# Performance work log

Measured on AMD Instinct MI355X. Metric: run time of the kernel, lower is better.

Reference implementation:

```python
import jax, jax.numpy as jnp
import numpy as np

B, S, DIM = 1, 2048, 1024
HEADS, KV_HEADS, DH = 16, 2, 64
GQ = HEADS // KV_HEADS
CBS = 64   # compress block size
SBS = 64   # selection block size
NUM_SEL = 8
WIN = 512  # sliding window size
NUM_MEM = 1
SCALE = DH ** -0.5
NEG = -jnp.finfo(jnp.float32).max


def setup_inputs():
    ks = jax.random.split(jax.random.key(0), 12)
    cdim = CBS * DH
    dim_inner = HEADS * DH
    dim_kv = KV_HEADS * DH
    p = lambda k, shape: jax.random.normal(k, shape, jnp.float32) * 0.02
    return {
        "x": jax.random.normal(ks[0], (B, S, DIM), jnp.float32),
        "rms_g": jnp.ones((DIM,), jnp.float32),
        "W_qkv": p(ks[1], (DIM, dim_inner + 2 * dim_kv)),
        "k_pos": p(ks[2], (KV_HEADS, CBS, DH)),
        "v_pos": p(ks[3], (KV_HEADS, CBS, DH)),
        "mem_kv": p(ks[4], (2, KV_HEADS, NUM_MEM, DH)),
        "kW1": p(ks[5], (cdim, cdim)), "kb1": jnp.zeros((cdim,), jnp.float32),
        "kW2": p(ks[6], (cdim, DH)), "kb2": jnp.zeros((DH,), jnp.float32),
        "vW1": p(ks[7], (cdim, cdim)), "vb1": jnp.zeros((cdim,), jnp.float32),
        "vW2": p(ks[8], (cdim, DH)), "vb2": jnp.zeros((DH,), jnp.float32),
        "W_comb": p(ks[9], (DIM, 3 * HEADS)),
        "b_comb": jnp.tile(jnp.array([-2.0, -2.0, 2.0], jnp.float32), HEADS),
        "W_out": p(ks[10], (HEADS * DH, DIM)),
    }


def _rot_half(u):
    v = u.reshape(u.shape[:-1] + (DH // 2, 2))
    return jnp.stack([-v[..., 1], v[..., 0]], axis=-1).reshape(u.shape)


def reference(x, rms_g, W_qkv, k_pos, v_pos, mem_kv, kW1, kb1, kW2, kb2,
              vW1, vb1, vW2, vb2, W_comb, b_comb, W_out):
    n_cb = S // CBS
    n_fb = S // SBS
    num_sel = min(NUM_SEL, n_cb)

    # RMSNorm
    xn = x * jax.lax.rsqrt(jnp.mean(x * x, -1, keepdims=True) + jnp.finfo(jnp.float32).eps) * rms_g

    qkv = xn @ W_qkv
    q, k, v = jnp.split(qkv, [HEADS * DH, (HEADS + KV_HEADS) * DH], axis=-1)
    q = q.reshape(B, S, HEADS, DH).transpose(0, 2, 1, 3)       # b h n d
    k = k.reshape(B, S, KV_HEADS, DH).transpose(0, 2, 1, 3)
    v = v.reshape(B, S, KV_HEADS, DH).transpose(0, 2, 1, 3)

    # ---- compressed branch: per-block MLP compression of K/V ----
    kc = (k + jnp.tile(k_pos, (1, n_cb, 1))[None]).reshape(B, KV_HEADS, n_cb, CBS * DH)
    vc = (v + jnp.tile(v_pos, (1, n_cb, 1))[None]).reshape(B, KV_HEADS, n_cb, CBS * DH)
    ck = jax.nn.relu(kc @ kW1 + kb1) @ kW2 + kb2               # b h w d
    cv = jax.nn.relu(vc @ vW1 + vb1) @ vW2 + vb2
    ck = jnp.concatenate([jnp.broadcast_to(mem_kv[0], (B, KV_HEADS, NUM_MEM, DH)), ck], axis=2)
    cv = jnp.concatenate([jnp.broadcast_to(mem_kv[1], (B, KV_HEADS, NUM_MEM, DH)), cv], axis=2)
    ck_seq = jnp.concatenate([jnp.full((NUM_MEM,), -1), (jnp.arange(n_cb) + 1) * CBS - 1])
    cmask = ck_seq[None, :] < jnp.arange(S)[:, None]           # [S, mem+n_cb]
    qg = q.reshape(B, KV_HEADS, GQ, S, DH)
    csim = jnp.einsum('bhgid,bhjd->bhgij', qg, ck) * SCALE
    csim = jnp.where(cmask, csim, NEG)
    c_out = jnp.einsum('bhgij,bhjd->bhgid', jax.nn.softmax(csim, -1), cv).reshape(B, HEADS, S, DH)

    # ---- rotary embedding (interleaved pairs, theta=10000) ----
    inv_freq = 1.0 / (10000.0 ** (jnp.arange(0, DH, 2, dtype=jnp.float32) / DH))
    freqs = jnp.repeat(jnp.arange(S, dtype=jnp.float32)[:, None] * inv_freq, 2, axis=-1)
    cos, sin = jnp.cos(freqs), jnp.sin(freqs)
    rq = q * cos + _rot_half(q) * sin
    rk = k * cos + _rot_half(k) * sin

    # ---- block selection from compressed attention scores ----
    imp = csim[..., NUM_MEM:].mean(axis=2)                     # mean over grouped queries: [B,KVH,S,n_cb]
    imp = jnp.concatenate([jnp.full(imp.shape[:-1] + (1,), -1000.0), imp], -1)
    imp = jax.nn.softmax(imp, -1)[..., 1:]
    sel_val, sel_idx = jax.lax.top_k(imp, num_sel)             # [B,KVH,S,sel]
    fmask = jnp.broadcast_to((sel_val > 1e-10)[..., None], (B, KV_HEADS, S, num_sel, SBS))
    diag_idx = jnp.broadcast_to((jnp.arange(S) // SBS)[None, None, :, None], (B, KV_HEADS, S, 1))
    sel_idx = jnp.concatenate([sel_idx, diag_idx], -1)         # append own (diagonal) block
    causal = jnp.tril(jnp.ones((SBS, SBS), bool))
    diag_mask = jnp.broadcast_to(jnp.tile(causal, (n_fb, 1))[None, None, :, None, :], (B, KV_HEADS, S, 1, SBS))
    fmask = jnp.concatenate([fmask, diag_mask], axis=-2).reshape(B, KV_HEADS, S, (num_sel + 1) * SBS)

    # ---- fine attention over gathered selected blocks ----
    fkb = rk.reshape(B, KV_HEADS, 1, n_fb, SBS, DH)
    fvb = v.reshape(B, KV_HEADS, 1, n_fb, SBS, DH)
    gi = sel_idx[..., None, None]                              # [B,KVH,S,sel+1,1,1]
    fk = jnp.take_along_axis(fkb, gi, axis=3).reshape(B, KV_HEADS, S, (num_sel + 1) * SBS, DH)
    fv = jnp.take_along_axis(fvb, gi, axis=3).reshape(B, KV_HEADS, S, (num_sel + 1) * SBS, DH)
    fqg = rq.reshape(B, KV_HEADS, GQ, S, DH)
    fsim = jnp.einsum('bhgid,bhijd->bhgij', fqg, fk) * SCALE
    fsim = jnp.where(fmask[:, :, None], fsim, NEG)
    f_out = jnp.einsum('bhgij,bhijd->bhgid', jax.nn.softmax(fsim, -1), fv).reshape(B, HEADS, S, DH)

    # ---- causal sliding window (exact window, look_backward=1) ----
    skf = jnp.repeat(rk, GQ, axis=1)
    svf = jnp.repeat(v, GQ, axis=1)
    nw = S // WIN
    kw = skf.reshape(B, HEADS, nw, WIN, DH)
    vw = svf.reshape(B, HEADS, nw, WIN, DH)
    kcat = jnp.concatenate([jnp.pad(kw, ((0, 0), (0, 0), (1, 0), (0, 0), (0, 0)))[:, :, :nw], kw], axis=3)
    vcat = jnp.concatenate([jnp.pad(vw, ((0, 0), (0, 0), (1, 0), (0, 0), (0, 0)))[:, :, :nw], vw], axis=3)
    qw = rq.reshape(B, HEADS, nw, WIN, DH)
    gq_pos = jnp.arange(nw)[:, None, None] * WIN + jnp.arange(WIN)[None, :, None]
    gk_pos = jnp.arange(nw)[:, None, None] * WIN - WIN + jnp.arange(2 * WIN)[None, None, :]
    smask = (gk_pos >= 0) & (gk_pos <= gq_pos) & (gq_pos - gk_pos <= WIN)
    ssim = jnp.where(smask, jnp.einsum('bhwid,bhwjd->bhwij', qw, kcat) * SCALE, NEG)
    s_out = jnp.einsum('bhwij,bhwjd->bhwid', jax.nn.softmax(ssim, -1), vcat).reshape(B, HEADS, S, DH)

    # ---- learned per-token, per-head strategy combination ----
    gates = jax.nn.sigmoid(xn @ W_comb + b_comb).reshape(B, S, HEADS, 3).transpose(0, 2, 1, 3)
    out = gates[..., 0:1] * c_out + gates[..., 1:2] * f_out + gates[..., 2:3] * s_out
    return out.transpose(0, 2, 1, 3).reshape(B, S, HEADS * DH) @ W_out
```

## Files before the change

kernel.cpp:

```cpp
#include <hip/hip_runtime.h>
#include <hip/hip_bf16.h>
#include <cstddef>
#include <cstdint>

#define S      2048
#define DIM    1024
#define HEADS  16
#define KVH    2
#define GQ     8
#define DH     64
#define CBS    64
#define SBS    64
#define NUMSEL 8
#define WIN    512
#define NCB    (S / CBS)
#define CDIM   (CBS * DH)
#define QKVC   (HEADS * DH + 2 * KVH * DH)
#define KOFF   (HEADS * DH)
#define VOFF   (HEADS * DH + KVH * DH)
#define SCALE  0.125f
#define RMS_EPS 1.1920928955078125e-07f

typedef __attribute__((ext_vector_type(8))) short bf16x8;
typedef __attribute__((ext_vector_type(4))) float f32x4;

__device__ inline short f2bs(float f) {
    __hip_bfloat16 b = __float2bfloat16(f);
    return *(short*)&b;
}

__device__ inline float wave_sum(float v) {
    for (int o = 32; o > 0; o >>= 1) v += __shfl_xor(v, o);
    return v;
}

__global__ __launch_bounds__(256) void rmsnorm_kernel(
        const float* __restrict__ x, const float* __restrict__ g,
        float* __restrict__ xn, __hip_bfloat16* __restrict__ xnb) {
    int s = blockIdx.x, tid = threadIdx.x;
    const float4* row = (const float4*)(x + (size_t)s * DIM);
    float4 v = row[tid];
    float ss = v.x * v.x + v.y * v.y + v.z * v.z + v.w * v.w;
    ss = wave_sum(ss);
    __shared__ float red[4];
    if ((tid & 63) == 0) red[tid >> 6] = ss;
    __syncthreads();
    float tot = red[0] + red[1] + red[2] + red[3];
    float sc = rsqrtf(tot / (float)DIM + RMS_EPS);
    float4 gg = ((const float4*)g)[tid];
    float4 o;
    o.x = v.x * sc * gg.x; o.y = v.y * sc * gg.y;
    o.z = v.z * sc * gg.z; o.w = v.w * sc * gg.w;
    ((float4*)(xn + (size_t)s * DIM))[tid] = o;
    size_t b = (size_t)s * DIM + tid * 4;
    xnb[b + 0] = __float2bfloat16(o.x);
    xnb[b + 1] = __float2bfloat16(o.y);
    xnb[b + 2] = __float2bfloat16(o.z);
    xnb[b + 3] = __float2bfloat16(o.w);
}

__global__ __launch_bounds__(256) void cast_bf16_kernel(
        const float* __restrict__ in, __hip_bfloat16* __restrict__ out, int n4) {
    int e = blockIdx.x * 256 + threadIdx.x;
    if (e >= n4) return;
    float4 v = ((const float4*)in)[e];
    out[4 * e + 0] = __float2bfloat16(v.x);
    out[4 * e + 1] = __float2bfloat16(v.y);
    out[4 * e + 2] = __float2bfloat16(v.z);
    out[4 * e + 3] = __float2bfloat16(v.w);
}

__global__ __launch_bounds__(256) void transpose_cast_kernel(
        const float* __restrict__ W, short* __restrict__ Wt, int K, int N) {
    __shared__ float tile[64][65];
    int n0 = blockIdx.x * 64, k0 = blockIdx.y * 64;
    int tid = threadIdx.x;
    #pragma unroll
    for (int e = 0; e < 16; e++) {
        int idx = tid + e * 256;
        int r = idx >> 6, c = idx & 63;
        float v = 0.f;
        if (n0 + c < N) v = W[(size_t)(k0 + r) * N + n0 + c];
        tile[r][c] = v;
    }
    __syncthreads();
    #pragma unroll
    for (int e = 0; e < 16; e++) {
        int idx = tid + e * 256;
        int r = idx >> 6, c = idx & 63;
        if (n0 + r < N)
            Wt[(size_t)(n0 + r) * K + k0 + c] = f2bs(tile[c][r]);
    }
}

__global__ __launch_bounds__(256) void cast_v_kernel(
        const float* __restrict__ qkv, short* __restrict__ vb) {
    int e = blockIdx.x * 256 + threadIdx.x;
    if (e >= S * KVH * DH / 4) return;
    int idx = e * 4;
    int tok = idx / (KVH * DH), rem = idx % (KVH * DH);
    float4 v = *(const float4*)(qkv + (size_t)tok * QKVC + VOFF + rem);
    vb[idx + 0] = f2bs(v.x);
    vb[idx + 1] = f2bs(v.y);
    vb[idx + 2] = f2bs(v.z);
    vb[idx + 3] = f2bs(v.w);
}

template <int BM, int BN, int WM, int WN, int ACT>
__global__ __launch_bounds__(256) void gemm_bt_kernel(
        const __hip_bfloat16* __restrict__ A, const short* __restrict__ Bt,
        const float* __restrict__ bias, float* __restrict__ C,
        int M, int N, int K) {
    constexpr int BK = 32;
    constexpr int TM = BM / (WM * 16);
    constexpr int TN = BN / (WN * 16);
    constexpr int LDK = BK + 8;
    __shared__ short As[BM][LDK];
    __shared__ short Bs[BN][LDK];
    int tid = threadIdx.x;
    int wave = tid >> 6, lane = tid & 63;
    int wm = wave % WM, wn = wave / WM;
    int m0 = wm * TM * 16, n0 = wn * TN * 16;
    int bm = blockIdx.y * BM, bn = blockIdx.x * BN;
    int lm = lane & 15, quad = lane >> 4;
    const short* Ash = (const short*)A;
    f32x4 acc[TM][TN] = {};
    for (int k0 = 0; k0 < K; k0 += BK) {
        #pragma unroll
        for (int e = 0; e < BM * BK / (256 * 8); e++) {
            int idx = (tid + e * 256) * 8;
            int r = idx >> 5, kk = idx & 31;
            *(bf16x8*)(&As[r][kk]) =
                *(const bf16x8*)(Ash + (size_t)(bm + r) * K + k0 + kk);
        }
        #pragma unroll
        for (int e = 0; e < BN * BK / (256 * 8); e++) {
            int idx = (tid + e * 256) * 8;
            int r = idx >> 5, kk = idx & 31;
            bf16x8 v = {};
            if (bn + r < N)
                v = *(const bf16x8*)(Bt + (size_t)(bn + r) * K + k0 + kk);
            *(bf16x8*)(&Bs[r][kk]) = v;
        }
        __syncthreads();
        bf16x8 af[TM], bf_[TN];
        #pragma unroll
        for (int i = 0; i < TM; i++)
            af[i] = *(const bf16x8*)(&As[m0 + i * 16 + lm][quad * 8]);
        #pragma unroll
        for (int j = 0; j < TN; j++)
            bf_[j] = *(const bf16x8*)(&Bs[n0 + j * 16 + lm][quad * 8]);
        #pragma unroll
        for (int i = 0; i < TM; i++)
            #pragma unroll
            for (int j = 0; j < TN; j++)
                acc[i][j] = __builtin_amdgcn_mfma_f32_16x16x32_bf16(
                    af[i], bf_[j], acc[i][j], 0, 0, 0);
        __syncthreads();
    }
    #pragma unroll
    for (int i = 0; i < TM; i++) {
        #pragma unroll
        for (int j = 0; j < TN; j++) {
            int gn = bn + n0 + j * 16 + lm;
            if (gn >= N) continue;
            #pragma unroll
            for (int r = 0; r < 4; r++) {
                int gm = bm + m0 + i * 16 + quad * 4 + r;
                float v = acc[i][j][r];
                if (bias) v += bias[gn];
                if (ACT == 2) v = 1.f / (1.f + expf(-v));
                C[(size_t)gm * N + gn] = v;
            }
        }
    }
}

template <int BM, int BN, int WM, int WN>
__global__ __launch_bounds__(256) void gemm_mfma_kernel(
        const __hip_bfloat16* __restrict__ A, const float* __restrict__ B,
        float* __restrict__ C, int M, int N, int K, int kslice) {
    constexpr int BK = 32;
    constexpr int TM = BM / (WM * 16);
    constexpr int TN = BN / (WN * 16);
    constexpr int LDK = BK + 8;
    constexpr int NB = BN * BK / 256;
    __shared__ __hip_bfloat16 As[BM][LDK];
    __shared__ __hip_bfloat16 Bs[BN][LDK];
    int tid = threadIdx.x;
    int wave = tid >> 6, lane = tid & 63;
    int wm = wave % WM, wn = wave / WM;
    int m0 = wm * TM * 16, n0 = wn * TN * 16;
    int bm = blockIdx.y * BM, bn = blockIdx.x * BN;
    int kbeg = blockIdx.z * kslice, kend = kbeg + kslice;
    int lm = lane & 15, quad = lane >> 4;
    f32x4 acc[TM][TN] = {};
    for (int k0 = kbeg; k0 < kend; k0 += BK) {
        #pragma unroll
        for (int e = 0; e < BM * BK / (256 * 8); e++) {
            int idx = (tid + e * 256) * 8;
            int r = idx >> 5, kk = idx & 31;
            *(bf16x8*)(&As[r][kk]) =
                *(const bf16x8*)(A + (size_t)(bm + r) * K + k0 + kk);
        }
        float tmpB[NB];
        #pragma unroll
        for (int e = 0; e < NB; e++) {
            int idx = tid + e * 256;
            int kk = idx / BN, n = idx % BN;
            tmpB[e] = B[(size_t)(k0 + kk) * N + bn + n];
        }
        #pragma unroll
        for (int e = 0; e < NB; e++) {
            int idx = tid + e * 256;
            int kk = idx / BN, n = idx % BN;
            Bs[n][kk] = __float2bfloat16(tmpB[e]);
        }
        __syncthreads();
        bf16x8 af[TM], bf_[TN];
        #pragma unroll
        for (int i = 0; i < TM; i++)
            af[i] = *(const bf16x8*)(&As[m0 + i * 16 + lm][quad * 8]);
        #pragma unroll
        for (int j = 0; j < TN; j++)
            bf_[j] = *(const bf16x8*)(&Bs[n0 + j * 16 + lm][quad * 8]);
        #pragma unroll
        for (int i = 0; i < TM; i++)
            #pragma unroll
            for (int j = 0; j < TN; j++)
                acc[i][j] = __builtin_amdgcn_mfma_f32_16x16x32_bf16(
                    af[i], bf_[j], acc[i][j], 0, 0, 0);
        __syncthreads();
    }
    size_t cbase = (size_t)blockIdx.z * M * N;
    #pragma unroll
    for (int i = 0; i < TM; i++) {
        #pragma unroll
        for (int j = 0; j < TN; j++) {
            int gn = bn + n0 + j * 16 + lm;
            #pragma unroll
            for (int r = 0; r < 4; r++) {
                int gm = bm + m0 + i * 16 + quad * 4 + r;
                C[cbase + (size_t)gm * N + gn] = acc[i][j][r];
            }
        }
    }
}

__global__ __launch_bounds__(256) void gemm_splitk_kernel(
        const float* __restrict__ A, const float* __restrict__ B,
        float* __restrict__ P, int M, int N, int K, int kslice) {
    const int BM = 64, BN = 64, BK = 16;
    __shared__ float As[BK][BM + 4];
    __shared__ float Bs[BK][BN];
    int bm = blockIdx.y * BM, bn = blockIdx.x * BN;
    int z = blockIdx.z;
    int kbeg = z * kslice, kend = kbeg + kslice;
    int tid = threadIdx.x;
    int tx = tid & 15, ty = tid >> 4;
    float acc[4][4] = {{0.f}};
    for (int k0 = kbeg; k0 < kend; k0 += BK) {
        #pragma unroll
        for (int e = 0; e < 4; e++) {
            int idx = tid + e * 256;
            int m = idx >> 4, kk = idx & 15;
            int gm = bm + m;
            As[kk][m] = (gm < M) ? A[(size_t)gm * K + k0 + kk] : 0.f;
        }
        #pragma unroll
        for (int e = 0; e < 4; e++) {
            int idx = tid + e * 256;
            int kk = idx >> 6, n = idx & 63;
            int gn = bn + n;
            Bs[kk][n] = (gn < N) ? B[(size_t)(k0 + kk) * N + gn] : 0.f;
        }
        __syncthreads();
        #pragma unroll
        for (int kk = 0; kk < BK; kk++) {
            float a[4], b[4];
            #pragma unroll
            for (int i = 0; i < 4; i++) a[i] = As[kk][ty * 4 + i];
            #pragma unroll
            for (int j = 0; j < 4; j++) b[j] = Bs[kk][tx * 4 + j];
            #pragma unroll
            for (int i = 0; i < 4; i++)
                #pragma unroll
                for (int j = 0; j < 4; j++) acc[i][j] += a[i] * b[j];
        }
        __syncthreads();
    }
    #pragma unroll
    for (int i = 0; i < 4; i++) {
        int gm = bm + ty * 4 + i;
        if (gm >= M) continue;
        #pragma unroll
        for (int j = 0; j < 4; j++) {
            int gn = bn + tx * 4 + j;
            if (gn >= N) continue;
            P[((size_t)z * M + gm) * N + gn] = acc[i][j];
        }
    }
}

template <int ACT>
__global__ __launch_bounds__(256) void reduce_splitk_kernel(
        const float* __restrict__ P, const float* __restrict__ bias,
        float* __restrict__ C, int MN, int N, int splits) {
    int e = blockIdx.x * 256 + threadIdx.x;
    if (e >= MN) return;
    float s = 0.f;
    for (int z = 0; z < splits; z++) s += P[(size_t)z * MN + e];
    s += bias[e % N];
    if (ACT == 1) s = fmaxf(s, 0.f);
    C[e] = s;
}

__global__ __launch_bounds__(256) void rotary_kernel(
        const float* __restrict__ qkv, short* __restrict__ rqb, short* __restrict__ rkb) {
    int s = blockIdx.x, tid = threadIdx.x;
    for (int p = tid; p < (HEADS + KVH) * (DH / 2); p += 256) {
        int t; const float* src; short* dst;
        if (p < HEADS * (DH / 2)) {
            int h = p >> 5; t = p & 31;
            src = qkv + (size_t)s * QKVC + h * DH + 2 * t;
            dst = rqb + (size_t)s * (HEADS * DH) + h * DH + 2 * t;
        } else {
            int pp = p - HEADS * (DH / 2);
            int h = pp >> 5; t = pp & 31;
            src = qkv + (size_t)s * QKVC + KOFF + h * DH + 2 * t;
            dst = rkb + (size_t)s * (KVH * DH) + h * DH + 2 * t;
        }
        float u0 = src[0], u1 = src[1];
        float freq = powf(10000.f, -((float)(2 * t) / (float)DH));
        float ang = (float)s * freq;
        float sn, cs;
        sincosf(ang, &sn, &cs);
        dst[0] = f2bs(u0 * cs - u1 * sn);
        dst[1] = f2bs(u1 * cs + u0 * sn);
    }
}

__global__ __launch_bounds__(256) void build_cmat_kernel(
        const float* __restrict__ qkv, const float* __restrict__ k_pos,
        const float* __restrict__ v_pos, __hip_bfloat16* __restrict__ kcm,
        __hip_bfloat16* __restrict__ vcm) {
    int r = blockIdx.x;
    int h = r >> 5, w = r & 31;
    for (int e = threadIdx.x; e < CDIM; e += 256) {
        int i = e >> 6, d = e & 63;
        size_t qb = (size_t)(w * CBS + i) * QKVC;
        kcm[(size_t)r * CDIM + e] =
            __float2bfloat16(qkv[qb + KOFF + h * DH + d] + k_pos[(h * CBS + i) * DH + d]);
        vcm[(size_t)r * CDIM + e] =
            __float2bfloat16(qkv[qb + VOFF + h * DH + d] + v_pos[(h * CBS + i) * DH + d]);
    }
}

__global__ __launch_bounds__(256) void assemble_kernel(
        const float* __restrict__ ckb, const float* __restrict__ cvb,
        const float* __restrict__ mem_kv, float* __restrict__ ck, float* __restrict__ cv,
        short* __restrict__ ck16, short* __restrict__ cv16) {
    int e = blockIdx.x * 256 + threadIdx.x;
    if (e >= KVH * (NCB + 1) * DH) return;
    int d = e & 63;
    int j = (e >> 6) % (NCB + 1);
    int h = e / ((NCB + 1) * DH);
    float kv, vv;
    if (j == 0) {
        kv = mem_kv[0 * KVH * DH + h * DH + d];
        vv = mem_kv[1 * KVH * DH + h * DH + d];
    } else {
        kv = ckb[((size_t)h * NCB + j - 1) * DH + d];
        vv = cvb[((size_t)h * NCB + j - 1) * DH + d];
    }
    ck[e] = kv; cv[e] = vv;
    ck16[e] = f2bs(kv); cv16[e] = f2bs(vv);
}

__global__ __launch_bounds__(64) void imp_kernel(
        const float* __restrict__ qkv, const float* __restrict__ ck,
        float* __restrict__ imp) {
    int kvh = blockIdx.x, s = blockIdx.y, t = threadIdx.x;
    __shared__ float qg[GQ * DH];
    __shared__ float ckl[NCB * 65];
    for (int e = t; e < GQ * DH; e += 64) {
        int g = e >> 6, d = e & 63;
        qg[e] = qkv[(size_t)s * QKVC + (kvh * GQ + g) * DH + d];
    }
    for (int e = t; e < NCB * DH; e += 64) {
        int w = e >> 6, d = e & 63;
        ckl[w * 65 + d] = ck[((size_t)kvh * (NCB + 1) + 1 + w) * DH + d];
    }
    __syncthreads();
    if (t < NCB) {
        int w = t;
        float val;
        if (w * CBS + CBS - 1 < s) {
            float acc = 0.f;
            #pragma unroll
            for (int g = 0; g < GQ; g++) {
                const float* qp = qg + g * DH;
                const float* cp = ckl + w * 65;
                #pragma unroll 16
                for (int d = 0; d < DH; d++) acc += qp[d] * cp[d];
            }
            val = acc * SCALE * (1.f / (float)GQ);
        } else {
            val = -INFINITY;
        }
        imp[((size_t)kvh * S + s) * NCB + w] = val;
    }
}

__global__ __launch_bounds__(256) void select_kernel(
        const float* __restrict__ imp, int* __restrict__ sel) {
    int idx = blockIdx.x * 256 + threadIdx.x;
    if (idx >= KVH * S) return;
    const float* row = imp + (size_t)idx * NCB;
    float p[NCB];
    float m = -1000.f;
    for (int w = 0; w < NCB; w++) { p[w] = row[w]; m = fmaxf(m, p[w]); }
    float z = expf(-1000.f - m);
    for (int w = 0; w < NCB; w++) { p[w] = expf(p[w] - m); z += p[w]; }
    float inv = 1.f / z;
    bool used[NCB];
    for (int w = 0; w < NCB; w++) used[w] = false;
    for (int i = 0; i < NUMSEL; i++) {
        int best = 0; float bv = -1.f;
        for (int w = 0; w < NCB; w++) {
            if (!used[w]) {
                float pw = p[w] * inv;
                if (pw > bv) { bv = pw; best = w; }
            }
        }
        used[best] = true;
        sel[(size_t)idx * NUMSEL + i] = (bv > 1e-10f) ? best : -1;
    }
}

__global__ __launch_bounds__(256) void cattn_kernel(
        const float* __restrict__ qkv, const short* __restrict__ ck16,
        const short* __restrict__ cv16, const float* __restrict__ gates,
        float* __restrict__ attn) {
    int h = blockIdx.x, qb = blockIdx.y;
    int kvh = h >> 3;
    int tid = threadIdx.x;
    int wv = tid >> 6, lane = tid & 63;
    int lm = lane & 15, quad = lane >> 4;
    __shared__ short Qb[64][72];
    __shared__ short Ks[64][72];
    __shared__ short Vt[64][72];
    __shared__ short Pb[64][72];
    for (int e = tid; e < 1024; e += 256) {
        int q = e >> 4, d4 = (e & 15) * 4;
        float4 v = *(const float4*)(qkv + (size_t)(qb * 64 + q) * QKVC + h * DH + d4);
        Qb[q][d4 + 0] = f2bs(v.x); Qb[q][d4 + 1] = f2bs(v.y);
        Qb[q][d4 + 2] = f2bs(v.z); Qb[q][d4 + 3] = f2bs(v.w);
    }
    for (int e = tid; e < 512; e += 256) {
        int c8 = e >> 6, j = e & 63;
        bf16x8 kv = {}, vv = {};
        if (j < NCB + 1) {
            kv = *(const bf16x8*)(ck16 + ((size_t)kvh * (NCB + 1) + j) * DH + c8 * 8);
            vv = *(const bf16x8*)(cv16 + ((size_t)kvh * (NCB + 1) + j) * DH + c8 * 8);
        }
        #pragma unroll
        for (int t = 0; t < 8; t++) {
            Ks[j][c8 * 8 + t] = kv[t];
            Vt[c8 * 8 + t][j] = vv[t];
        }
    }
    __syncthreads();
    bf16x8 aq0 = *(const bf16x8*)&Qb[wv * 16 + lm][quad * 8];
    bf16x8 aq1 = *(const bf16x8*)&Qb[wv * 16 + lm][32 + quad * 8];
    int vismax = (qb < NCB) ? qb : NCB;
    f32x4 sc[4];
    #pragma unroll
    for (int t = 0; t < 4; t++) {
        bf16x8 bk0 = *(const bf16x8*)&Ks[t * 16 + lm][quad * 8];
        bf16x8 bk1 = *(const bf16x8*)&Ks[t * 16 + lm][32 + quad * 8];
        f32x4 s4 = {0.f, 0.f, 0.f, 0.f};
        s4 = __builtin_amdgcn_mfma_f32_16x16x32_bf16(aq0, bk0, s4, 0, 0, 0);
        s4 = __builtin_amdgcn_mfma_f32_16x16x32_bf16(aq1, bk1, s4, 0, 0, 0);
        sc[t] = s4;
    }
    float l[4];
    float pr[4][4];
    #pragma unroll
    for (int r = 0; r < 4; r++) {
        float mx = -INFINITY;
        #pragma unroll
        for (int t = 0; t < 4; t++) {
            int jj = t * 16 + lm;
            bool vis = (jj == 0) || (jj <= vismax);
            float v = vis ? sc[t][r] * SCALE : -INFINITY;
            sc[t][r] = v;
            mx = fmaxf(mx, v);
        }
        #pragma unroll
        for (int o = 1; o < 16; o <<= 1) mx = fmaxf(mx, __shfl_xor(mx, o));
        float sum = 0.f;
        #pragma unroll
        for (int t = 0; t < 4; t++) {
            float p = expf(sc[t][r] - mx);
            pr[r][t] = p;
            sum += p;
        }
        #pragma unroll
        for (int o = 1; o < 16; o <<= 1) sum += __shfl_xor(sum, o);
        l[r] = sum;
    }
    #pragma unroll
    for (int r = 0; r < 4; r++)
        #pragma unroll
        for (int t = 0; t < 4; t++)
            Pb[wv * 16 + quad * 4 + r][t * 16 + lm] = f2bs(pr[r][t]);
    __syncthreads();
    bf16x8 ap0 = *(const bf16x8*)&Pb[wv * 16 + lm][quad * 8];
    bf16x8 ap1 = *(const bf16x8*)&Pb[wv * 16 + lm][32 + quad * 8];
    f32x4 oacc[4];
    #pragma unroll
    for (int t = 0; t < 4; t++) {
        bf16x8 bv0 = *(const bf16x8*)&Vt[t * 16 + lm][quad * 8];
        bf16x8 bv1 = *(const bf16x8*)&Vt[t * 16 + lm][32 + quad * 8];
        f32x4 a = {0.f, 0.f, 0.f, 0.f};
        a = __builtin_amdgcn_mfma_f32_16x16x32_bf16(ap0, bv0, a, 0, 0, 0);
        a = __builtin_amdgcn_mfma_f32_16x16x32_bf16(ap1, bv1, a, 0, 0, 0);
        oacc[t] = a;
    }
    #pragma unroll
    for (int r = 0; r < 4; r++) {
        int spos = qb * 64 + wv * 16 + quad * 4 + r;
        float g0 = gates[((size_t)spos * HEADS + h) * 3 + 0];
        float f = g0 / l[r];
        #pragma unroll
        for (int t = 0; t < 4; t++)
            attn[(size_t)spos * (HEADS * DH) + h * DH + t * 16 + lm] = oacc[t][r] * f;
    }
}

__global__ __launch_bounds__(64, 4) void fattn_kernel(
        const short* __restrict__ rqb, const short* __restrict__ rkb,
        const short* __restrict__ vb, const int* __restrict__ sel,
        const float* __restrict__ gates, float* __restrict__ attn) {
    int kvh = blockIdx.x, s = blockIdx.y;
    int lane = threadIdx.x;
    int lm = lane & 15, quad = lane >> 4;
    __shared__ short Vt[64][68];
    __shared__ short Pb[16][68];
    const short* qp = rqb + (size_t)s * (HEADS * DH) + (size_t)(kvh * 8 + (lm & 7)) * DH;
    bf16x8 aq0 = *(const bf16x8*)(qp + quad * 8);
    bf16x8 aq1 = *(const bf16x8*)(qp + 32 + quad * 8);
    int bl[9];
    {
        const int4* sp = (const int4*)(sel + ((size_t)kvh * S + s) * NUMSEL);
        int4 s0 = sp[0], s1 = sp[1];
        bl[0] = s0.x; bl[1] = s0.y; bl[2] = s0.z; bl[3] = s0.w;
        bl[4] = s1.x; bl[5] = s1.y; bl[6] = s1.z; bl[7] = s1.w;
        bl[8] = s >> 6;
    }
    float m[4], l[4];
    f32x4 oacc[4];
    #pragma unroll
    for (int r = 0; r < 4; r++) {
        m[r] = -INFINITY; l[r] = 0.f;
        oacc[r] = (f32x4){0.f, 0.f, 0.f, 0.f};
    }
    for (int i = 0; i < 9; i++) {
        int w = bl[i];
        if (i < NUMSEL && w < 0) continue;
        const short* vp = vb + ((size_t)(w * SBS + lane) * KVH + kvh) * DH;
        bf16x8 vv[8];
        #pragma unroll
        for (int r = 0; r < 8; r++) vv[r] = *(const bf16x8*)(vp + r * 8);
        f32x4 sc[4];
        #pragma unroll
        for (int t = 0; t < 4; t++) {
            const short* kp = rkb + ((size_t)(w * SBS + t * 16 + lm) * KVH + kvh) * DH;
            bf16x8 bk0 = *(const bf16x8*)(kp + quad * 8);
            bf16x8 bk1 = *(const bf16x8*)(kp + 32 + quad * 8);
            f32x4 s4 = {0.f, 0.f, 0.f, 0.f};
            s4 = __builtin_amdgcn_mfma_f32_16x16x32_bf16(aq0, bk0, s4, 0, 0, 0);
            s4 = __builtin_amdgcn_mfma_f32_16x16x32_bf16(aq1, bk1, s4, 0, 0, 0);
            sc[t] = s4;
        }
        #pragma unroll
        for (int r = 0; r < 8; r++)
            #pragma unroll
            for (int t = 0; t < 8; t++) Vt[r * 8 + t][lane] = vv[r][t];
        float pr[4][4];
        bool diag = (i == NUMSEL);
        #pragma unroll
        for (int r = 0; r < 4; r++) {
            float mx = -INFINITY;
            #pragma unroll
            for (int t = 0; t < 4; t++) {
                int jj = t * 16 + lm;
                bool vis = !diag || (jj <= (s & 63));
                float v = vis ? sc[t][r] * SCALE : -INFINITY;
                sc[t][r] = v;
                mx = fmaxf(mx, v);
            }
            #pragma unroll
            for (int o = 1; o < 16; o <<= 1) mx = fmaxf(mx, __shfl_xor(mx, o));
            float mn = fmaxf(m[r], mx);
            float al = __expf(m[r] - mn);
            float sum = 0.f;
            #pragma unroll
            for (int t = 0; t < 4; t++) {
                float p = __expf(sc[t][r] - mn);
                pr[r][t] = p;
                sum += p;
            }
            #pragma unroll
            for (int o = 1; o < 16; o <<= 1) sum += __shfl_xor(sum, o);
            l[r] = l[r] * al + sum;
            m[r] = mn;
            #pragma unroll
            for (int t = 0; t < 4; t++) oacc[t][r] *= al;
        }
        #pragma unroll
        for (int r = 0; r < 4; r++)
            #pragma unroll
            for (int t = 0; t < 4; t++)
                Pb[quad * 4 + r][t * 16 + lm] = f2bs(pr[r][t]);
        asm volatile("s_waitcnt lgkmcnt(0)" ::: "memory");
        bf16x8 ap0 = *(const bf16x8*)&Pb[lm][quad * 8];
        bf16x8 ap1 = *(const bf16x8*)&Pb[lm][32 + quad * 8];
        #pragma unroll
        for (int t = 0; t < 4; t++) {
            bf16x8 bv0 = *(const bf16x8*)&Vt[t * 16 + lm][quad * 8];
            bf16x8 bv1 = *(const bf16x8*)&Vt[t * 16 + lm][32 + quad * 8];
            oacc[t] = __builtin_amdgcn_mfma_f32_16x16x32_bf16(ap0, bv0, oacc[t], 0, 0, 0);
            oacc[t] = __builtin_amdgcn_mfma_f32_16x16x32_bf16(ap1, bv1, oacc[t], 0, 0, 0);
        }
    }
    if (quad < 2) {
        #pragma unroll
        for (int r = 0; r < 4; r++) {
            int head = kvh * 8 + quad * 4 + r;
            float fac = gates[((size_t)s * HEADS + head) * 3 + 1] / l[r];
            #pragma unroll
            for (int t = 0; t < 4; t++)
                attn[(size_t)s * (HEADS * DH) + head * DH + t * 16 + lm]
                    += oacc[t][r] * fac;
        }
    }
}

__global__ __launch_bounds__(256) void sattn_kernel(
        const short* __restrict__ rqb, const short* __restrict__ rkb,
        const short* __restrict__ vb, const float* __restrict__ gates,
        float* __restrict__ attn) {
    int h = blockIdx.x, qb = blockIdx.y;
    int kvh = h >> 3;
    int tid = threadIdx.x;
    int wv = tid >> 6, lane = tid & 63;
    int lm = lane & 15, quad = lane >> 4;
    __shared__ short Vt[64][72];
    __shared__ short Pb[64][72];
    const short* qp = rqb + (size_t)(qb * 64 + wv * 16 + lm) * (HEADS * DH) + h * DH;
    bf16x8 aq0 = *(const bf16x8*)(qp + quad * 8);
    bf16x8 aq1 = *(const bf16x8*)(qp + 32 + quad * 8);
    int myrow = wv * 16 + quad * 4;
    float m[4], l[4];
    f32x4 oacc[4];
    #pragma unroll
    for (int r = 0; r < 4; r++) { m[r] = -INFINITY; l[r] = 0.f; }
    #pragma unroll
    for (int t = 0; t < 4; t++) oacc[t] = (f32x4){0.f, 0.f, 0.f, 0.f};
    for (int c = 0; c < 9; c++) {
        int kb = qb * 64 - WIN + c * 64;
        if (kb < 0) continue;
        for (int e = tid; e < 512; e += 256) {
            int c8 = e >> 6, j = e & 63;
            bf16x8 vv = *(const bf16x8*)(vb + ((size_t)(kb + j) * KVH + kvh) * DH + c8 * 8);
            #pragma unroll
            for (int t = 0; t < 8; t++) Vt[c8 * 8 + t][j] = vv[t];
        }
        f32x4 sc[4];
        #pragma unroll
        for (int t = 0; t < 4; t++) {
            const short* kp = rkb + ((size_t)(kb + t * 16 + lm) * KVH + kvh) * DH;
            bf16x8 bk0 = *(const bf16x8*)(kp + quad * 8);
            bf16x8 bk1 = *(const bf16x8*)(kp + 32 + quad * 8);
            f32x4 s4 = {0.f, 0.f, 0.f, 0.f};
            s4 = __builtin_amdgcn_mfma_f32_16x16x32_bf16(aq0, bk0, s4, 0, 0, 0);
            s4 = __builtin_amdgcn_mfma_f32_16x16x32_bf16(aq1, bk1, s4, 0, 0, 0);
            sc[t] = s4;
        }
        float pr[4][4];
        #pragma unroll
        for (int r = 0; r < 4; r++) {
            int row = myrow + r;
            float mx = -INFINITY;
            #pragma unroll
            for (int t = 0; t < 4; t++) {
                int jj = t * 16 + lm;
                bool vis = true;
                if (c == 0) vis = (jj >= row);
                if (c == 8) vis = (jj <= row);
                float v = vis ? sc[t][r] * SCALE : -INFINITY;
                sc[t][r] = v;
                mx = fmaxf(mx, v);
            }
            #pragma unroll
            for (int o = 1; o < 16; o <<= 1) mx = fmaxf(mx, __shfl_xor(mx, o));
            float mn = fmaxf(m[r], mx);
            float al = expf(m[r] - mn);
            float sum = 0.f;
            #pragma unroll
            for (int t = 0; t < 4; t++) {
                float p = expf(sc[t][r] - mn);
                pr[r][t] = p;
                sum += p;
            }
            #pragma unroll
            for (int o = 1; o < 16; o <<= 1) sum += __shfl_xor(sum, o);
            l[r] = l[r] * al + sum;
            m[r] = mn;
            #pragma unroll
            for (int t = 0; t < 4; t++) oacc[t][r] *= al;
        }
        __syncthreads();
        #pragma unroll
        for (int r = 0; r < 4; r++)
            #pragma unroll
            for (int t = 0; t < 4; t++)
                Pb[myrow + r][t * 16 + lm] = f2bs(pr[r][t]);
        __syncthreads();
        bf16x8 ap0 = *(const bf16x8*)&Pb[wv * 16 + lm][quad * 8];
        bf16x8 ap1 = *(const bf16x8*)&Pb[wv * 16 + lm][32 + quad * 8];
        #pragma unroll
        for (int t = 0; t < 4; t++) {
            bf16x8 bv0 = *(const bf16x8*)&Vt[t * 16 + lm][quad * 8];
            bf16x8 bv1 = *(const bf16x8*)&Vt[t * 16 + lm][32 + quad * 8];
            oacc[t] = __builtin_amdgcn_mfma_f32_16x16x32_bf16(ap0, bv0, oacc[t], 0, 0, 0);
            oacc[t] = __builtin_amdgcn_mfma_f32_16x16x32_bf16(ap1, bv1, oacc[t], 0, 0, 0);
        }
        __syncthreads();
    }
    #pragma unroll
    for (int r = 0; r < 4; r++) {
        int spos = qb * 64 + myrow + r;
        float g2 = gates[((size_t)spos * HEADS + h) * 3 + 2];
        float f = g2 / l[r];
        #pragma unroll
        for (int t = 0; t < 4; t++)
            attn[(size_t)spos * (HEADS * DH) + h * DH + t * 16 + lm] += oacc[t][r] * f;
    }
}

extern "C" void kernel_launch(void* const* d_in, const int* in_sizes, int n_in,
                              void* d_out, int out_size, void* d_ws, size_t ws_size,
                              hipStream_t stream) {
    const float* x      = (const float*)d_in[0];
    const float* rms_g  = (const float*)d_in[1];
    const float* W_qkv  = (const float*)d_in[2];
    const float* k_pos  = (const float*)d_in[3];
    const float* v_pos  = (const float*)d_in[4];
    const float* mem_kv = (const float*)d_in[5];
    const float* kW1    = (const float*)d_in[6];
    const float* kb1    = (const float*)d_in[7];
    const float* kW2    = (const float*)d_in[8];
    const float* kb2    = (const float*)d_in[9];
    const float* vW1    = (const float*)d_in[10];
    const float* vb1    = (const float*)d_in[11];
    const float* vW2    = (const float*)d_in[12];
    const float* vb2    = (const float*)d_in[13];
    const float* W_comb = (const float*)d_in[14];
    const float* b_comb = (const float*)d_in[15];
    const float* W_out  = (const float*)d_in[16];
    float* out = (float*)d_out;

    float* ws    = (float*)d_ws;
    float* xn    = ws;
    float* qkv   = xn    + (size_t)S * DIM;
    short* rqb   = (short*)(qkv + (size_t)S * QKVC);
    short* rkb   = (short*)((float*)rqb + 1048576);
    float* R     = (float*)rkb + 131072;
    float* ck    = R     + 1048576;
    float* cv    = ck    + (size_t)KVH * (NCB + 1) * DH;
    short* ck16  = (short*)(cv + (size_t)KVH * (NCB + 1) * DH);
    short* cv16  = (short*)((float*)ck16 + 2112);
    float* imp   = (float*)cv16 + 2112;
    float* gates = imp   + (size_t)KVH * S * NCB;
    float* attn  = gates + (size_t)S * HEADS * 3;
    int*   sel   = (int*)(attn + (size_t)S * HEADS * DH);
    float* WT    = attn + (size_t)S * HEADS * DH + 8192;
    short* wqkvT = (short*)WT;
    short* woutT = (short*)(WT + 655360);
    short* wcombT= (short*)(WT + 655360 + 524288);

    __hip_bfloat16* xnb   = (__hip_bfloat16*)R;
    __hip_bfloat16* kcmb  = (__hip_bfloat16*)R;
    __hip_bfloat16* vcmb  = (__hip_bfloat16*)(R + 131072);
    float* khid  = R + 262144;
    float* vhid  = R + 524288;
    float* ckb   = R + 786432;
    float* cvb   = R + 790528;
    __hip_bfloat16* attnb = (__hip_bfloat16*)R;
    short* vbb   = (short*)imp;
    float* partW1 = attn;
    float* partW2 = imp;

    transpose_cast_kernel<<<dim3(QKVC / 64, DIM / 64), 256, 0, stream>>>(W_qkv, wqkvT, DIM, QKVC);
    transpose_cast_kernel<<<dim3(DIM / 64, DIM / 64), 256, 0, stream>>>(W_out, woutT, DIM, DIM);
    transpose_cast_kernel<<<dim3(1, DIM / 64), 256, 0, stream>>>(W_comb, wcombT, DIM, HEADS * 3);
    rmsnorm_kernel<<<S, 256, 0, stream>>>(x, rms_g, xn, xnb);
    gemm_bt_kernel<64, 64, 2, 2, 0><<<dim3(QKVC / 64, S / 64), 256, 0, stream>>>(
        xnb, wqkvT, nullptr, qkv, S, QKVC, DIM);
    gemm_bt_kernel<64, 64, 2, 2, 2><<<dim3(1, S / 64), 256, 0, stream>>>(
        xnb, wcombT, b_comb, gates, S, HEADS * 3, DIM);
    rotary_kernel<<<S, 256, 0, stream>>>(qkv, rqb, rkb);
    build_cmat_kernel<<<KVH * NCB, 256, 0, stream>>>(qkv, k_pos, v_pos, kcmb, vcmb);
    gemm_mfma_kernel<64, 128, 1, 4><<<dim3(CDIM / 128, 1, 8), 256, 0, stream>>>(
        kcmb, kW1, partW1, 64, CDIM, CDIM, CDIM / 8);
    reduce_splitk_kernel<1><<<(64 * CDIM + 255) / 256, 256, 0, stream>>>(
        partW1, kb1, khid, 64 * CDIM, CDIM, 8);
    gemm_splitk_kernel<<<dim3(1, 1, 32), 256, 0, stream>>>(khid, kW2, partW2, 64, DH, CDIM, CDIM / 32);
    reduce_splitk_kernel<0><<<(64 * DH + 255) / 256, 256, 0, stream>>>(partW2, kb2, ckb, 64 * DH, DH, 32);
    gemm_mfma_kernel<64, 128, 1, 4><<<dim3(CDIM / 128, 1, 8), 256, 0, stream>>>(
        vcmb, vW1, partW1, 64, CDIM, CDIM, CDIM / 8);
    reduce_splitk_kernel<1><<<(64 * CDIM + 255) / 256, 256, 0, stream>>>(
        partW1, vb1, vhid, 64 * CDIM, CDIM, 8);
    gemm_splitk_kernel<<<dim3(1, 1, 32), 256, 0, stream>>>(vhid, vW2, partW2, 64, DH, CDIM, CDIM / 32);
    reduce_splitk_kernel<0><<<(64 * DH + 255) / 256, 256, 0, stream>>>(partW2, vb2, cvb, 64 * DH, DH, 32);
    assemble_kernel<<<(KVH * (NCB + 1) * DH + 255) / 256, 256, 0, stream>>>(
        ckb, cvb, mem_kv, ck, cv, ck16, cv16);
    imp_kernel<<<dim3(KVH, S), 64, 0, stream>>>(qkv, ck, imp);
    select_kernel<<<(KVH * S + 255) / 256, 256, 0, stream>>>(imp, sel);
    cast_v_kernel<<<(S * KVH * DH / 4 + 255) / 256, 256, 0, stream>>>(qkv, vbb);
    cattn_kernel<<<dim3(HEADS, S / 64), 256, 0, stream>>>(qkv, ck16, cv16, gates, attn);
    fattn_kernel<<<dim3(KVH, S), 64, 0, stream>>>(rqb, rkb, vbb, sel, gates, attn);
    sattn_kernel<<<dim3(HEADS, S / 64), 256, 0, stream>>>(rqb, rkb, vbb, gates, attn);
    cast_bf16_kernel<<<(S * HEADS * DH / 4 + 255) / 256, 256, 0, stream>>>(
        attn, attnb, S * HEADS * DH / 4);
    gemm_bt_kernel<64, 64, 2, 2, 0><<<dim3(DIM / 64, S / 64), 256, 0, stream>>>(
        attnb, woutT, nullptr, out, S, DIM, DIM);
}
```

Before: 547.2 us.

## Prefetch K/V tiles in fine attention and double-buffer V in sliding attention

The fine (selected-block) attention kernel now software-pipelines its loop, loading the next block's K and V fragments into registers while the current block is processed. The loop is fully unrolled and the launch-bounds occupancy hint drops from 4 to 2 to leave room for the extra registers. The sliding-window kernel double-buffers its transposed V tile in shared memory, cutting three barriers per chunk to one plus an lgkmcnt wait, since each wave only reads its own rows of the P buffer. Several expf calls become the faster __expf, trading a little accuracy and occupancy for hidden load latency and fewer synchronisations.

```diff
diff --git a/kernel.cpp b/kernel.cpp
--- a/kernel.cpp
+++ b/kernel.cpp
@@ -502,7 +502,7 @@
         float sum = 0.f;
         #pragma unroll
         for (int t = 0; t < 4; t++) {
-            float p = expf(sc[t][r] - mx);
+            float p = __expf(sc[t][r] - mx);
             pr[r][t] = p;
             sum += p;
         }
@@ -539,7 +539,7 @@
     }
 }
 
-__global__ __launch_bounds__(64, 4) void fattn_kernel(
+__global__ __launch_bounds__(64, 2) void fattn_kernel(
         const short* __restrict__ rqb, const short* __restrict__ rkb,
         const short* __restrict__ vb, const int* __restrict__ sel,
         const float* __restrict__ gates, float* __restrict__ attn) {
@@ -566,30 +566,50 @@
         m[r] = -INFINITY; l[r] = 0.f;
         oacc[r] = (f32x4){0.f, 0.f, 0.f, 0.f};
     }
+    bf16x8 kpre[2][4][2];
+    bf16x8 vpre[2][8];
+    {
+        int w0 = bl[0] < 0 ? 0 : bl[0];
+        #pragma unroll
+        for (int t = 0; t < 4; t++) {
+            const short* kp = rkb + ((size_t)(w0 * SBS + t * 16 + lm) * KVH + kvh) * DH;
+            kpre[0][t][0] = *(const bf16x8*)(kp + quad * 8);
+            kpre[0][t][1] = *(const bf16x8*)(kp + 32 + quad * 8);
+        }
+        const short* vp = vb + ((size_t)(w0 * SBS + lane) * KVH + kvh) * DH;
+        #pragma unroll
+        for (int r = 0; r < 8; r++) vpre[0][r] = *(const bf16x8*)(vp + r * 8);
+    }
+    #pragma unroll
     for (int i = 0; i < 9; i++) {
-        int w = bl[i];
-        if (i < NUMSEL && w < 0) continue;
-        const short* vp = vb + ((size_t)(w * SBS + lane) * KVH + kvh) * DH;
-        bf16x8 vv[8];
-        #pragma unroll
-        for (int r = 0; r < 8; r++) vv[r] = *(const bf16x8*)(vp + r * 8);
+        const int p = i & 1;
+        const int pn = p ^ 1;
+        if (i < 8) {
+            int wn = bl[i + 1] < 0 ? 0 : bl[i + 1];
+            #pragma unroll
+            for (int t = 0; t < 4; t++) {
+                const short* kp = rkb + ((size_t)(wn * SBS + t * 16 + lm) * KVH + kvh) * DH;
+                kpre[pn][t][0] = *(const bf16x8*)(kp + quad * 8);
+                kpre[pn][t][1] = *(const bf16x8*)(kp + 32 + quad * 8);
+            }
+            const short* vp = vb + ((size_t)(wn * SBS + lane) * KVH + kvh) * DH;
+            #pragma unroll
+            for (int r = 0; r < 8; r++) vpre[pn][r] = *(const bf16x8*)(vp + r * 8);
+        }
+        if (i < 8 && bl[i] < 0) continue;
+        #pragma unroll
+        for (int r = 0; r < 8; r++)
+            #pragma unroll
+            for (int t = 0; t < 8; t++) Vt[r * 8 + t][lane] = vpre[p][r][t];
         f32x4 sc[4];
         #pragma unroll
         for (int t = 0; t < 4; t++) {
-            const short* kp = rkb + ((size_t)(w * SBS + t * 16 + lm) * KVH + kvh) * DH;
-            bf16x8 bk0 = *(const bf16x8*)(kp + quad * 8);
-            bf16x8 bk1 = *(const bf16x8*)(kp + 32 + quad * 8);
             f32x4 s4 = {0.f, 0.f, 0.f, 0.f};
-            s4 = __builtin_amdgcn_mfma_f32_16x16x32_bf16(aq0, bk0, s4, 0, 0, 0);
-            s4 = __builtin_amdgcn_mfma_f32_16x16x32_bf16(aq1, bk1, s4, 0, 0, 0);
+            s4 = __builtin_amdgcn_mfma_f32_16x16x32_bf16(aq0, kpre[p][t][0], s4, 0, 0, 0);
+            s4 = __builtin_amdgcn_mfma_f32_16x16x32_bf16(aq1, kpre[p][t][1], s4, 0, 0, 0);
             sc[t] = s4;
         }
-        #pragma unroll
-        for (int r = 0; r < 8; r++)
-            #pragma unroll
-            for (int t = 0; t < 8; t++) Vt[r * 8 + t][lane] = vv[r][t];
-        float pr[4][4];
-        bool diag = (i == NUMSEL);
+        bool diag = (i == 8);
         #pragma unroll
         for (int r = 0; r < 4; r++) {
             float mx = -INFINITY;
@@ -608,9 +628,9 @@
             float sum = 0.f;
             #pragma unroll
             for (int t = 0; t < 4; t++) {
-                float p = __expf(sc[t][r] - mn);
-                pr[r][t] = p;
-                sum += p;
+                float pv_ = __expf(sc[t][r] - mn);
+                sc[t][r] = pv_;
+                sum += pv_;
             }
             #pragma unroll
             for (int o = 1; o < 16; o <<= 1) sum += __shfl_xor(sum, o);
@@ -623,7 +643,7 @@
         for (int r = 0; r < 4; r++)
             #pragma unroll
             for (int t = 0; t < 4; t++)
-                Pb[quad * 4 + r][t * 16 + lm] = f2bs(pr[r][t]);
+                Pb[quad * 4 + r][t * 16 + lm] = f2bs(sc[t][r]);
         asm volatile("s_waitcnt lgkmcnt(0)" ::: "memory");
         bf16x8 ap0 = *(const bf16x8*)&Pb[lm][quad * 8];
         bf16x8 ap1 = *(const bf16x8*)&Pb[lm][32 + quad * 8];
@@ -657,27 +677,26 @@
     int tid = threadIdx.x;
     int wv = tid >> 6, lane = tid & 63;
     int lm = lane & 15, quad = lane >> 4;
-    __shared__ short Vt[64][72];
+    __shared__ short Vt[2][64][72];
     __shared__ short Pb[64][72];
     const short* qp = rqb + (size_t)(qb * 64 + wv * 16 + lm) * (HEADS * DH) + h * DH;
     bf16x8 aq0 = *(const bf16x8*)(qp + quad * 8);
     bf16x8 aq1 = *(const bf16x8*)(qp + 32 + quad * 8);
     int myrow = wv * 16 + quad * 4;
+    int j0 = tid & 63, c80 = tid >> 6;
     float m[4], l[4];
     f32x4 oacc[4];
     #pragma unroll
     for (int r = 0; r < 4; r++) { m[r] = -INFINITY; l[r] = 0.f; }
     #pragma unroll
     for (int t = 0; t < 4; t++) oacc[t] = (f32x4){0.f, 0.f, 0.f, 0.f};
+    int nc = 0;
     for (int c = 0; c < 9; c++) {
         int kb = qb * 64 - WIN + c * 64;
         if (kb < 0) continue;
-        for (int e = tid; e < 512; e += 256) {
-            int c8 = e >> 6, j = e & 63;
-            bf16x8 vv = *(const bf16x8*)(vb + ((size_t)(kb + j) * KVH + kvh) * DH + c8 * 8);
-            #pragma unroll
-            for (int t = 0; t < 8; t++) Vt[c8 * 8 + t][j] = vv[t];
-        }
+        const short* vp = vb + ((size_t)(kb + j0) * KVH + kvh) * DH;
+        bf16x8 vv0 = *(const bf16x8*)(vp + c80 * 8);
+        bf16x8 vv1 = *(const bf16x8*)(vp + (c80 + 4) * 8);
         f32x4 sc[4];
         #pragma unroll
         for (int t = 0; t < 4; t++) {
@@ -689,7 +708,12 @@
             s4 = __builtin_amdgcn_mfma_f32_16x16x32_bf16(aq1, bk1, s4, 0, 0, 0);
             sc[t] = s4;
         }
-        float pr[4][4];
+        short* vtb = &Vt[nc & 1][0][0];
+        #pragma unroll
+        for (int t = 0; t < 8; t++) vtb[(size_t)(c80 * 8 + t) * 72 + j0] = vv0[t];
+        #pragma unroll
+        for (int t = 0; t < 8; t++) vtb[(size_t)((c80 + 4) * 8 + t) * 72 + j0] = vv1[t];
+        __syncthreads();
         #pragma unroll
         for (int r = 0; r < 4; r++) {
             int row = myrow + r;
@@ -707,13 +731,13 @@
             #pragma unroll
             for (int o = 1; o < 16; o <<= 1) mx = fmaxf(mx, __shfl_xor(mx, o));
             float mn = fmaxf(m[r], mx);
-            float al = expf(m[r] - mn);
+            float al = __expf(m[r] - mn);
             float sum = 0.f;
             #pragma unroll
             for (int t = 0; t < 4; t++) {
-                float p = expf(sc[t][r] - mn);
-                pr[r][t] = p;
-                sum += p;
+                float pv_ = __expf(sc[t][r] - mn);
+                sc[t][r] = pv_;
+                sum += pv_;
             }
             #pragma unroll
             for (int o = 1; o < 16; o <<= 1) sum += __shfl_xor(sum, o);
@@ -722,23 +746,22 @@
             #pragma unroll
             for (int t = 0; t < 4; t++) oacc[t][r] *= al;
         }
-        __syncthreads();
         #pragma unroll
         for (int r = 0; r < 4; r++)
             #pragma unroll
             for (int t = 0; t < 4; t++)
-                Pb[myrow + r][t * 16 + lm] = f2bs(pr[r][t]);
-        __syncthreads();
+                Pb[myrow + r][t * 16 + lm] = f2bs(sc[t][r]);
+        asm volatile("s_waitcnt lgkmcnt(0)" ::: "memory");
         bf16x8 ap0 = *(const bf16x8*)&Pb[wv * 16 + lm][quad * 8];
         bf16x8 ap1 = *(const bf16x8*)&Pb[wv * 16 + lm][32 + quad * 8];
         #pragma unroll
         for (int t = 0; t < 4; t++) {
-            bf16x8 bv0 = *(const bf16x8*)&Vt[t * 16 + lm][quad * 8];
-            bf16x8 bv1 = *(const bf16x8*)&Vt[t * 16 + lm][32 + quad * 8];
+            bf16x8 bv0 = *(const bf16x8*)(vtb + (size_t)(t * 16 + lm) * 72 + quad * 8);
+            bf16x8 bv1 = *(const bf16x8*)(vtb + (size_t)(t * 16 + lm) * 72 + 32 + quad * 8);
             oacc[t] = __builtin_amdgcn_mfma_f32_16x16x32_bf16(ap0, bv0, oacc[t], 0, 0, 0);
             oacc[t] = __builtin_amdgcn_mfma_f32_16x16x32_bf16(ap1, bv1, oacc[t], 0, 0, 0);
         }
-        __syncthreads();
+        nc++;
     }
     #pragma unroll
     for (int r = 0; r < 4; r++) {
```

Result: slower. 559.9 us (+2.3%).
